# Kernel optimization log

Hardware: AMD Instinct MI355X
Metric: run time of the kernel (lower is better)

## Reference

```python
import jax, jax.numpy as jnp
import numpy as np

ALPHA = 0.2  # LeakyReLU negative slope
NEG_INF = -9e15  # matches torch's -9000000000000000.0


def setup_inputs() -> dict:
    key = jax.random.key(0)
    k1, k2, k3, k4 = jax.random.split(key, 4)
    B, T, N, F_in, D = 4, 32, 512, 128, 128
    h = jax.random.normal(k1, (B, T, N, F_in), dtype=jnp.float32)
    adj = jax.random.randint(k2, (N, N), 0, 2, dtype=jnp.int32)
    # params: W ~ Linear(in_dim, out_dim, bias=False); a ~ Linear(2*out_dim, 1, bias=False)
    W = jax.random.normal(k3, (F_in, D), dtype=jnp.float32) * 0.05
    a = jax.random.normal(k4, (2 * D,), dtype=jnp.float32) * 0.05
    return {"h": h, "adj": adj, "W": W, "a": a}


def reference(h, adj, W, a):
    # h: (B,T,N,F_in), adj: (N,N), W: (F_in,D), a: (2D,)
    D = W.shape[1]
    Wh = jnp.einsum('btnf,fd->btnd', h, W)  # (B,T,N,D)
    # a . [Wh_i ; Wh_j] == a_src . Wh_i + a_dst . Wh_j -- avoids (N,N,2D) concat
    a_src, a_dst = a[:D], a[D:]
    e_src = Wh @ a_src  # (B,T,N)
    e_dst = Wh @ a_dst  # (B,T,N)
    e = jax.nn.leaky_relu(e_src[..., :, None] + e_dst[..., None, :], ALPHA)  # (B,T,N,N)
    e = jnp.where(adj > 0, e, jnp.float32(NEG_INF))
    attention = jax.nn.softmax(e, axis=-1)  # dropout is identity at eval
    h_prime = jnp.einsum('btij,btjd->btid', attention, Wh)  # (B,T,N,D)
    return h_prime
```

## Files before the change

kernel.cpp:

```cpp
#include <hip/hip_runtime.h>
#include <math.h>

typedef __attribute__((ext_vector_type(8))) short bf16x8;
typedef __attribute__((ext_vector_type(4))) float f32x4;

#define MFMA(a, b, c) __builtin_amdgcn_mfma_f32_16x16x32_bf16(a, b, c, 0, 0, 0)

constexpr int GN = 128;
constexpr int NN = 512;
constexpr int FD = 128;
#define LOG2E 1.4426950408889634f

__device__ inline unsigned rne_top16(float x) {
    unsigned u = __float_as_uint(x);
    return u + 0x7fffu + ((u >> 16) & 1u);
}
__device__ inline unsigned pack_top16(unsigned e1, unsigned e0) {
    return __builtin_amdgcn_perm(e1, e0, 0x07060302u);
}
__device__ inline void gload16(const void* g, void* l) {
    __builtin_amdgcn_global_load_lds(
        (const __attribute__((address_space(1))) unsigned*)g,
        (__attribute__((address_space(3))) unsigned*)l, 16, 0, 0);
}

__global__ __launch_bounds__(256) void prep_kernel(
    const int* __restrict__ adj, const float* __restrict__ W,
    unsigned* __restrict__ mask, unsigned short* __restrict__ wsHi,
    unsigned short* __restrict__ wsLo)
{
    const int b = blockIdx.x, t = threadIdx.x;
    if (b < 32) {
        const int wi = b * 256 + t;
        const int row = wi >> 4, wo = wi & 15;
        const int* p = adj + row * NN + wo * 32;
        unsigned m = 0;
        #pragma unroll
        for (int q = 0; q < 32; q += 4) {
            int4 v = *(const int4*)&p[q];
            m |= (v.x > 0 ? 1u : 0u) << q;
            m |= (v.y > 0 ? 1u : 0u) << (q + 1);
            m |= (v.z > 0 ? 1u : 0u) << (q + 2);
            m |= (v.w > 0 ? 1u : 0u) << (q + 3);
        }
        mask[wi] = m;
    } else {
        const int base = (b - 32) * 512 + t * 2;
        #pragma unroll
        for (int q = 0; q < 2; ++q) {
            const int pos = base + q;
            const int idx = pos & 7, lane = (pos >> 3) & 63, cn = pos >> 9;
            const int kk = cn >> 3, nb = cn & 7;
            const int k = kk * 32 + ((lane >> 4) & 3) * 8 + idx;
            const int d = nb * 16 + (lane & 15);
            const float wv = W[k * FD + d];
            const unsigned u = __float_as_uint(wv);
            wsHi[pos] = (unsigned short)(u >> 16);
            wsLo[pos] = (unsigned short)(rne_top16(
                            wv - __uint_as_float(u & 0xffff0000u)) >> 16);
        }
    }
}

__global__ __launch_bounds__(256, 2) void whb_kernel(
    const float* __restrict__ h, const float* __restrict__ a,
    const unsigned short* __restrict__ wsHi, const unsigned short* __restrict__ wsLo,
    unsigned short* __restrict__ whtHi,
    float* __restrict__ esrc, float* __restrict__ edst)
{
    __shared__ __attribute__((aligned(16))) unsigned short sW[32768];

    const int bid = blockIdx.x;
    const int xcd = bid & 7, slot = bid >> 3;
    const int g = xcd + 8 * (slot >> 2);
    const int jt = slot & 3;
    const int t = threadIdx.x, lane = t & 63, w = t >> 6;
    const int i0r = jt * 128;
    const int q8 = (lane >> 4) * 8;
    const float* hg = h + (size_t)(g * NN) * FD;

    float4 hv[16];
    #pragma unroll
    for (int kk = 0; kk < 4; ++kk)
        #pragma unroll
        for (int mt = 0; mt < 2; ++mt) {
            const float* src = hg + (size_t)(i0r + w * 32 + mt * 16 + (lane & 15)) * FD
                             + kk * 32 + q8;
            hv[(kk * 2 + mt) * 2 + 0] = *(const float4*)src;
            hv[(kk * 2 + mt) * 2 + 1] = *(const float4*)(src + 4);
        }
    for (int q = t; q < 2048; q += 256) {
        gload16(&wsHi[q * 8], &sW[q * 8]);
        gload16(&wsLo[q * 8], &sW[16384 + q * 8]);
    }
    __syncthreads();

    f32x4 acc[2][8];
    #pragma unroll
    for (int mt = 0; mt < 2; ++mt)
        #pragma unroll
        for (int nb = 0; nb < 8; ++nb) acc[mt][nb] = (f32x4){0.f, 0.f, 0.f, 0.f};

    #pragma unroll
    for (int kk = 0; kk < 4; ++kk) {
        bf16x8 ah[2], al[2];
        #pragma unroll
        for (int mt = 0; mt < 2; ++mt) {
            const float4 f0 = hv[(kk * 2 + mt) * 2 + 0];
            const float4 f1 = hv[(kk * 2 + mt) * 2 + 1];
            const float xs[8] = {f0.x, f0.y, f0.z, f0.w, f1.x, f1.y, f1.z, f1.w};
            union { bf16x8 v; unsigned u[4]; } H, L;
            #pragma unroll
            for (int j = 0; j < 4; ++j) {
                const unsigned e0 = __float_as_uint(xs[2 * j]);
                const unsigned e1 = __float_as_uint(xs[2 * j + 1]);
                H.u[j] = pack_top16(e1, e0);
                const unsigned l0 = rne_top16(xs[2*j]   - __uint_as_float(e0 & 0xffff0000u));
                const unsigned l1 = rne_top16(xs[2*j+1] - __uint_as_float(e1 & 0xffff0000u));
                L.u[j] = pack_top16(l1, l0);
            }
            ah[mt] = H.v; al[mt] = L.v;
        }
        #pragma unroll
        for (int nb = 0; nb < 8; ++nb) {
            const bf16x8 bh = *(const bf16x8*)&sW[((kk * 8 + nb) * 64 + lane) * 8];
            const bf16x8 bl = *(const bf16x8*)&sW[16384 + ((kk * 8 + nb) * 64 + lane) * 8];
            #pragma unroll
            for (int mt = 0; mt < 2; ++mt) {
                acc[mt][nb] = MFMA(al[mt], bh, acc[mt][nb]);
                acc[mt][nb] = MFMA(ah[mt], bl, acc[mt][nb]);
                acc[mt][nb] = MFMA(ah[mt], bh, acc[mt][nb]);
            }
        }
    }

    float av[8], bv[8];
    #pragma unroll
    for (int nb = 0; nb < 8; ++nb) {
        av[nb] = a[nb * 16 + (lane & 15)];
        bv[nb] = a[FD + nb * 16 + (lane & 15)];
    }
    #pragma unroll
    for (int mt = 0; mt < 2; ++mt)
        #pragma unroll
        for (int r = 0; r < 4; ++r) {
            float ps = 0.f, pd = 0.f;
            #pragma unroll
            for (int nb = 0; nb < 8; ++nb) {
                ps += acc[mt][nb][r] * av[nb];
                pd += acc[mt][nb][r] * bv[nb];
            }
            #pragma unroll
            for (int off = 1; off <= 8; off <<= 1) {
                ps += __shfl_xor(ps, off);
                pd += __shfl_xor(pd, off);
            }
            if ((lane & 15) == 0) {
                const int row = g * NN + i0r + w * 32 + mt * 16 + (lane >> 4) * 4 + r;
                esrc[row] = ps;
                edst[row] = pd;
            }
        }

    unsigned short* sT = sW;
    const size_t gbase = (size_t)g * 65536 + (size_t)jt * 16384;
    const int ib = 4 * ((lane >> 4) & 1);

    __syncthreads();
    #pragma unroll
    for (int mt = 0; mt < 2; ++mt) {
        const int lp2 = (lane & 15) + 16 * (mt * 2 + (lane >> 5));
        #pragma unroll
        for (int nb = 0; nb < 8; ++nb) {
            const int off = ((w * 8 + nb) * 64 + lp2) * 8 + ib;
            const unsigned r0 = rne_top16(acc[mt][nb][0]);
            const unsigned r1 = rne_top16(acc[mt][nb][1]);
            const unsigned r2 = rne_top16(acc[mt][nb][2]);
            const unsigned r3 = rne_top16(acc[mt][nb][3]);
            *(uint2*)&sT[off] = make_uint2(pack_top16(r1, r0), pack_top16(r3, r2));
        }
    }
    __syncthreads();
    for (int q = t; q < 2048; q += 256)
        *(float4*)&whtHi[gbase + q * 8] = *(const float4*)&sT[q * 8];
}

__global__ __launch_bounds__(256, 2) void attn_kernel(
    const unsigned short* __restrict__ whtHi,
    const float* __restrict__ esrc, const float* __restrict__ edst,
    const unsigned* __restrict__ mask, float* __restrict__ out)
{
    __shared__ __attribute__((aligned(16))) float eds[NN];
    __shared__ unsigned maskS[128 * 17];
    __shared__ __attribute__((aligned(16))) unsigned short cHi[2][8192];

    const int bid = blockIdx.x;
    const int xcd = bid & 7, slot = bid >> 3;
    const int g = xcd + 8 * (slot >> 2);
    const int it = slot & 3;
    const int t = threadIdx.x, lane = t & 63, w = t >> 6;
    const int i0 = it * 128;
    const int q8 = (lane >> 4) * 8;
    const int l15 = lane & 15;

    eds[t]       = edst[g * NN + t] * LOG2E;
    eds[t + 256] = edst[g * NN + 256 + t] * LOG2E;
    for (int q = t; q < 2048; q += 256) {
        const int row = q >> 4, wo = q & 15;
        maskS[row * 17 + wo] = mask[(i0 + row) * 16 + wo];
    }

    const int rloc0 = w * 32 + l15;
    const int rloc1 = rloc0 + 16;
    const float s0 = esrc[g * NN + i0 + rloc0] * LOG2E;
    const float s1 = esrc[g * NN + i0 + rloc1] * LOG2E;

    const size_t gbase = (size_t)g * 65536;
    for (int q = t; q < 1024; q += 256)
        gload16(&whtHi[gbase + q * 8], &cHi[0][q * 8]);
    __syncthreads();

    f32x4 acc[2][8];
    #pragma unroll
    for (int mt = 0; mt < 2; ++mt)
        #pragma unroll
        for (int nb = 0; nb < 8; ++nb) acc[mt][nb] = (f32x4){0.f, 0.f, 0.f, 0.f};
    float lsum0 = 0.f, lsum1 = 0.f;

    for (int c2 = 0; c2 < 8; ++c2) {
        const int cur = c2 & 1, nxt = cur ^ 1;
        if (c2 < 7) {
            const size_t gb = gbase + (size_t)(c2 + 1) * 8192;
            for (int q = t; q < 1024; q += 256)
                gload16(&whtHi[gb + q * 8], &cHi[nxt][q * 8]);
        }
        const unsigned short* __restrict__ bHi = &cHi[cur][0];
        #pragma unroll
        for (int kl = 0; kl < 2; ++kl) {
            const int kk = c2 * 2 + kl;
            const float* ep = &eds[kk * 32 + q8];
            const float4 ed0 = *(const float4*)ep;
            const float4 ed1 = *(const float4*)(ep + 4);
            const float ev[8] = {ed0.x, ed0.y, ed0.z, ed0.w, ed1.x, ed1.y, ed1.z, ed1.w};
            const unsigned mw0 = maskS[rloc0 * 17 + kk] >> q8;
            const unsigned mw1 = maskS[rloc1 * 17 + kk] >> q8;

            union { bf16x8 v; unsigned u[4]; } H0, H1;
            unsigned uh0[8], uh1[8];
            #pragma unroll
            for (int i = 0; i < 8; ++i) {
                const float z0 = s0 + ev[i];
                float p0 = __builtin_amdgcn_exp2f(fmaxf(z0, 0.2f * z0));
                p0 = ((mw0 >> i) & 1u) ? p0 : 0.f;
                const unsigned u0 = __float_as_uint(p0) & 0xffff0000u;
                lsum0 += __uint_as_float(u0);
                uh0[i] = u0;
                const float z1 = s1 + ev[i];
                float p1 = __builtin_amdgcn_exp2f(fmaxf(z1, 0.2f * z1));
                p1 = ((mw1 >> i) & 1u) ? p1 : 0.f;
                const unsigned u1 = __float_as_uint(p1) & 0xffff0000u;
                lsum1 += __uint_as_float(u1);
                uh1[i] = u1;
            }
            #pragma unroll
            for (int j = 0; j < 4; ++j) {
                H0.u[j] = pack_top16(uh0[2*j+1], uh0[2*j]);
                H1.u[j] = pack_top16(uh1[2*j+1], uh1[2*j]);
            }
            #pragma unroll
            for (int nb = 0; nb < 8; ++nb) {
                const bf16x8 bh = *(const bf16x8*)&bHi[((kl * 8 + nb) * 64 + lane) * 8];
                acc[0][nb] = MFMA(H0.v, bh, acc[0][nb]);
                acc[1][nb] = MFMA(H1.v, bh, acc[1][nb]);
            }
        }
        __syncthreads();
    }

    lsum0 += __shfl_xor(lsum0, 16); lsum0 += __shfl_xor(lsum0, 32);
    lsum1 += __shfl_xor(lsum1, 16); lsum1 += __shfl_xor(lsum1, 32);

    #pragma unroll
    for (int r = 0; r < 4; ++r) {
        const int rr = (lane >> 4) * 4 + r;
        const float rl0 = 1.0f / __shfl(lsum0, rr);
        const float rl1 = 1.0f / __shfl(lsum1, rr);
        const int row0 = g * NN + i0 + w * 32 + rr;
        const int row1 = row0 + 16;
        #pragma unroll
        for (int nb = 0; nb < 8; ++nb) {
            out[row0 * FD + nb * 16 + l15] = acc[0][nb][r] * rl0;
            out[row1 * FD + nb * 16 + l15] = acc[1][nb][r] * rl1;
        }
    }
}

extern "C" void kernel_launch(void* const* d_in, const int* in_sizes, int n_in,
                              void* d_out, int out_size, void* d_ws, size_t ws_size,
                              hipStream_t stream) {
    const float* h   = (const float*)d_in[0];
    const int*   adj = (const int*)d_in[1];
    const float* W   = (const float*)d_in[2];
    const float* a   = (const float*)d_in[3];
    float* out = (float*)d_out;

    unsigned short* whtHi = (unsigned short*)d_ws;
    float* esrc = (float*)(whtHi + (size_t)GN * 65536);
    float* edst = esrc + GN * NN;
    unsigned* mask = (unsigned*)(edst + GN * NN);
    unsigned short* wsHi = (unsigned short*)(mask + 8192);
    unsigned short* wsLo = wsHi + 16384;

    prep_kernel<<<64, 256, 0, stream>>>(adj, W, mask, wsHi, wsLo);
    whb_kernel<<<512, 256, 0, stream>>>(h, a, wsHi, wsLo, whtHi, esrc, edst);
    attn_kernel<<<512, 256, 0, stream>>>(whtHi, esrc, edst, mask, out);
}
```

Before: 115.5 us.

## Fold prep kernel into projection kernel and compute softmax row sums via MFMA

Removes the separate prep kernel launch. Each projection block now builds one row of the adjacency bitmask with ballots and converts W into the hi/lo bf16 split directly in shared memory. Every block therefore redoes the W split, adding global reads of W, in exchange for one fewer launch and one fewer round trip through global memory. In the attention kernel, the per-thread scalar sum of truncated probabilities is replaced by an extra MFMA against a ones column, which drops the masking, adds and shuffles from the inner loop at the cost of two extra MFMAs per k-step.

```diff
diff --git a/kernel.cpp b/kernel.cpp
--- a/kernel.cpp
+++ b/kernel.cpp
@@ -24,49 +24,12 @@
         (__attribute__((address_space(3))) unsigned*)l, 16, 0, 0);
 }
 
-__global__ __launch_bounds__(256) void prep_kernel(
-    const int* __restrict__ adj, const float* __restrict__ W,
-    unsigned* __restrict__ mask, unsigned short* __restrict__ wsHi,
-    unsigned short* __restrict__ wsLo)
-{
-    const int b = blockIdx.x, t = threadIdx.x;
-    if (b < 32) {
-        const int wi = b * 256 + t;
-        const int row = wi >> 4, wo = wi & 15;
-        const int* p = adj + row * NN + wo * 32;
-        unsigned m = 0;
-        #pragma unroll
-        for (int q = 0; q < 32; q += 4) {
-            int4 v = *(const int4*)&p[q];
-            m |= (v.x > 0 ? 1u : 0u) << q;
-            m |= (v.y > 0 ? 1u : 0u) << (q + 1);
-            m |= (v.z > 0 ? 1u : 0u) << (q + 2);
-            m |= (v.w > 0 ? 1u : 0u) << (q + 3);
-        }
-        mask[wi] = m;
-    } else {
-        const int base = (b - 32) * 512 + t * 2;
-        #pragma unroll
-        for (int q = 0; q < 2; ++q) {
-            const int pos = base + q;
-            const int idx = pos & 7, lane = (pos >> 3) & 63, cn = pos >> 9;
-            const int kk = cn >> 3, nb = cn & 7;
-            const int k = kk * 32 + ((lane >> 4) & 3) * 8 + idx;
-            const int d = nb * 16 + (lane & 15);
-            const float wv = W[k * FD + d];
-            const unsigned u = __float_as_uint(wv);
-            wsHi[pos] = (unsigned short)(u >> 16);
-            wsLo[pos] = (unsigned short)(rne_top16(
-                            wv - __uint_as_float(u & 0xffff0000u)) >> 16);
-        }
-    }
-}
-
 __global__ __launch_bounds__(256, 2) void whb_kernel(
     const float* __restrict__ h, const float* __restrict__ a,
-    const unsigned short* __restrict__ wsHi, const unsigned short* __restrict__ wsLo,
+    const int* __restrict__ adj, const float* __restrict__ W,
     unsigned short* __restrict__ whtHi,
-    float* __restrict__ esrc, float* __restrict__ edst)
+    float* __restrict__ esrc, float* __restrict__ edst,
+    unsigned* __restrict__ mask)
 {
     __shared__ __attribute__((aligned(16))) unsigned short sW[32768];
 
@@ -89,9 +52,43 @@
             hv[(kk * 2 + mt) * 2 + 0] = *(const float4*)src;
             hv[(kk * 2 + mt) * 2 + 1] = *(const float4*)(src + 4);
         }
-    for (int q = t; q < 2048; q += 256) {
-        gload16(&wsHi[q * 8], &sW[q * 8]);
-        gload16(&wsLo[q * 8], &sW[16384 + q * 8]);
+
+    {
+        const int pred0 = adj[bid * NN + t] > 0;
+        const int pred1 = adj[bid * NN + 256 + t] > 0;
+        const unsigned long long m0 = __ballot(pred0);
+        const unsigned long long m1 = __ballot(pred1);
+        if (lane == 0) {
+            mask[bid * 16 + 2 * w]     = (unsigned)m0;
+            mask[bid * 16 + 8 + 2 * w] = (unsigned)m1;
+        } else if (lane == 1) {
+            mask[bid * 16 + 2 * w + 1]     = (unsigned)(m0 >> 32);
+            mask[bid * 16 + 8 + 2 * w + 1] = (unsigned)(m1 >> 32);
+        }
+    }
+
+    #pragma unroll
+    for (int grp = 0; grp < 8; ++grp) {
+        const int p8 = grp * 256 + t;
+        const int lanep = p8 & 63, cn = p8 >> 6;
+        const int kks = cn >> 3, nbs = cn & 7;
+        const int kbase = kks * 32 + ((lanep >> 4) & 3) * 8;
+        const int d = nbs * 16 + (lanep & 15);
+        unsigned hi[8], lo[8];
+        #pragma unroll
+        for (int idx = 0; idx < 8; ++idx) {
+            const float wv = W[(kbase + idx) * FD + d];
+            const unsigned u = __float_as_uint(wv);
+            hi[idx] = u;
+            lo[idx] = rne_top16(wv - __uint_as_float(u & 0xffff0000u));
+        }
+        uint4 H4, L4;
+        H4.x = pack_top16(hi[1], hi[0]); H4.y = pack_top16(hi[3], hi[2]);
+        H4.z = pack_top16(hi[5], hi[4]); H4.w = pack_top16(hi[7], hi[6]);
+        L4.x = pack_top16(lo[1], lo[0]); L4.y = pack_top16(lo[3], lo[2]);
+        L4.z = pack_top16(lo[5], lo[4]); L4.w = pack_top16(lo[7], lo[6]);
+        *(uint4*)&sW[p8 * 8]         = H4;
+        *(uint4*)&sW[16384 + p8 * 8] = L4;
     }
     __syncthreads();
 
@@ -215,6 +212,13 @@
     const float s0 = esrc[g * NN + i0 + rloc0] * LOG2E;
     const float s1 = esrc[g * NN + i0 + rloc1] * LOG2E;
 
+    union { bf16x8 v; unsigned short s[8]; } bo;
+    {
+        const unsigned short oneb = (l15 == 0) ? (unsigned short)0x3f80 : (unsigned short)0;
+        #pragma unroll
+        for (int j = 0; j < 8; ++j) bo.s[j] = oneb;
+    }
+
     const size_t gbase = (size_t)g * 65536;
     for (int q = t; q < 1024; q += 256)
         gload16(&whtHi[gbase + q * 8], &cHi[0][q * 8]);
@@ -225,7 +229,8 @@
     for (int mt = 0; mt < 2; ++mt)
         #pragma unroll
         for (int nb = 0; nb < 8; ++nb) acc[mt][nb] = (f32x4){0.f, 0.f, 0.f, 0.f};
-    float lsum0 = 0.f, lsum1 = 0.f;
+    f32x4 accS0 = (f32x4){0.f, 0.f, 0.f, 0.f};
+    f32x4 accS1 = (f32x4){0.f, 0.f, 0.f, 0.f};
 
     for (int c2 = 0; c2 < 8; ++c2) {
         const int cur = c2 & 1, nxt = cur ^ 1;
@@ -252,15 +257,11 @@
                 const float z0 = s0 + ev[i];
                 float p0 = __builtin_amdgcn_exp2f(fmaxf(z0, 0.2f * z0));
                 p0 = ((mw0 >> i) & 1u) ? p0 : 0.f;
-                const unsigned u0 = __float_as_uint(p0) & 0xffff0000u;
-                lsum0 += __uint_as_float(u0);
-                uh0[i] = u0;
+                uh0[i] = __float_as_uint(p0);
                 const float z1 = s1 + ev[i];
                 float p1 = __builtin_amdgcn_exp2f(fmaxf(z1, 0.2f * z1));
                 p1 = ((mw1 >> i) & 1u) ? p1 : 0.f;
-                const unsigned u1 = __float_as_uint(p1) & 0xffff0000u;
-                lsum1 += __uint_as_float(u1);
-                uh1[i] = u1;
+                uh1[i] = __float_as_uint(p1);
             }
             #pragma unroll
             for (int j = 0; j < 4; ++j) {
@@ -273,19 +274,17 @@
                 acc[0][nb] = MFMA(H0.v, bh, acc[0][nb]);
                 acc[1][nb] = MFMA(H1.v, bh, acc[1][nb]);
             }
+            accS0 = MFMA(H0.v, bo.v, accS0);
+            accS1 = MFMA(H1.v, bo.v, accS1);
         }
         __syncthreads();
     }
 
-    lsum0 += __shfl_xor(lsum0, 16); lsum0 += __shfl_xor(lsum0, 32);
-    lsum1 += __shfl_xor(lsum1, 16); lsum1 += __shfl_xor(lsum1, 32);
-
     #pragma unroll
     for (int r = 0; r < 4; ++r) {
-        const int rr = (lane >> 4) * 4 + r;
-        const float rl0 = 1.0f / __shfl(lsum0, rr);
-        const float rl1 = 1.0f / __shfl(lsum1, rr);
-        const int row0 = g * NN + i0 + w * 32 + rr;
+        const float rl0 = 1.0f / __shfl(accS0[r], lane & 48);
+        const float rl1 = 1.0f / __shfl(accS1[r], lane & 48);
+        const int row0 = g * NN + i0 + w * 32 + (lane >> 4) * 4 + r;
         const int row1 = row0 + 16;
         #pragma unroll
         for (int nb = 0; nb < 8; ++nb) {
@@ -308,10 +307,7 @@
     float* esrc = (float*)(whtHi + (size_t)GN * 65536);
     float* edst = esrc + GN * NN;
     unsigned* mask = (unsigned*)(edst + GN * NN);
-    unsigned short* wsHi = (unsigned short*)(mask + 8192);
-    unsigned short* wsLo = wsHi + 16384;
-
-    prep_kernel<<<64, 256, 0, stream>>>(adj, W, mask, wsHi, wsLo);
-    whb_kernel<<<512, 256, 0, stream>>>(h, a, wsHi, wsLo, whtHi, esrc, edst);
+
+    whb_kernel<<<512, 256, 0, stream>>>(h, a, adj, W, whtHi, esrc, edst, mask);
     attn_kernel<<<512, 256, 0, stream>>>(whtHi, esrc, edst, mask, out);
 }
```

New measurement: 113.8 us. Within noise of the previous version (-1.5%).
